# Optimization experiments

Measured on AMD Instinct MI355X. Metric: run time of the kernel, lower is better.

The kernel has to match this reference:

```python
import jax, jax.numpy as jnp
import numpy as np

OBS, ACT, HID, P, B = 128, 32, 256, 64, 4096
EPS = 1e-5


def _block(x, W, b, g, be, act=True):
    # x: [B, P, Din]; W: [P, Din, Dout]; b/g/be: [P, Dout]
    y = jnp.einsum('bpi,pio->bpo', x, W) + b
    # GroupNorm with one group per sub-policy: normalize over Dout per (b, p)
    mu = jnp.mean(y, axis=-1, keepdims=True)
    var = jnp.var(y, axis=-1, keepdims=True)
    y = (y - mu) * jax.lax.rsqrt(var + EPS) * g + be
    return jax.nn.elu(y) if act else y


def setup_inputs() -> dict:
    key = jax.random.key(0)
    ks = jax.random.split(key, 17)
    s = 0.05
    return {
        'observation': jax.random.normal(ks[0], (B, OBS), dtype=jnp.float32),
        'W1': jax.random.normal(ks[1], (P, OBS, HID), dtype=jnp.float32) * s,
        'b1': jax.random.normal(ks[2], (P, HID), dtype=jnp.float32) * s,
        'g1': jnp.ones((P, HID), dtype=jnp.float32),
        'be1': jnp.zeros((P, HID), dtype=jnp.float32),
        'W2': jax.random.normal(ks[3], (P, HID, HID), dtype=jnp.float32) * s,
        'b2': jax.random.normal(ks[4], (P, HID), dtype=jnp.float32) * s,
        'g2': jnp.ones((P, HID), dtype=jnp.float32),
        'be2': jnp.zeros((P, HID), dtype=jnp.float32),
        'W3': jax.random.normal(ks[5], (P, HID, HID), dtype=jnp.float32) * s,
        'b3': jax.random.normal(ks[6], (P, HID), dtype=jnp.float32) * s,
        'g3': jnp.ones((P, HID), dtype=jnp.float32),
        'be3': jnp.zeros((P, HID), dtype=jnp.float32),
        'W4': jax.random.normal(ks[7], (P, HID, ACT), dtype=jnp.float32) * s,
        'b4': jax.random.normal(ks[8], (P, ACT), dtype=jnp.float32) * s,
        'g4': jnp.ones((P, ACT), dtype=jnp.float32),
        'be4': jnp.zeros((P, ACT), dtype=jnp.float32),
    }


def reference(observation, W1, b1, g1, be1, W2, b2, g2, be2,
              W3, b3, g3, be3, W4, b4, g4, be4):
    # broadcast observation to each sub-policy: [B, P, OBS]
    x = jnp.broadcast_to(observation[:, None, :], (observation.shape[0], P, OBS))
    x = _block(x, W1, b1, g1, be1, act=True)
    x = _block(x, W2, b2, g2, be2, act=True)
    x = _block(x, W3, b3, g3, be3, act=True)
    x = _block(x, W4, b4, g4, be4, act=False)
    return x  # [B, P, ACT] action logits
```

## Files before the change

kernel.cpp:

```cpp
#include <hip/hip_runtime.h>

#define B_    4096
#define P_    64
#define OBS_  128
#define HID_  256
#define ACTD_ 32

typedef __attribute__((ext_vector_type(8)))  __bf16 bf16x8;
typedef __attribute__((ext_vector_type(2)))  __bf16 bf16x2_t;
typedef __attribute__((ext_vector_type(2)))  float  f32x2;
typedef __attribute__((ext_vector_type(4)))  float  f32x4;
typedef __attribute__((ext_vector_type(16))) float  f32x16;

#define XSTRIDE 264

#define WS1 0L
#define WS2 2097152L
#define WS3 6291456L
#define WS4 10485760L

#if defined(__has_builtin)
#if __has_builtin(__builtin_amdgcn_cvt_pk_bf16_f32)
#define HAVE_CVT_PK_BF16 1
#endif
#endif
#ifndef HAVE_CVT_PK_BF16
#define HAVE_CVT_PK_BF16 0
#endif

__device__ __forceinline__ unsigned short f2bf(float x) {
    unsigned u = __builtin_bit_cast(unsigned, x);
    u = (u + 0x7fffu + ((u >> 16) & 1u)) >> 16;
    return (unsigned short)u;
}

__device__ __forceinline__ unsigned pack_bf16_rne(float a, float b) {
#if HAVE_CVT_PK_BF16
    bf16x2_t p = __builtin_amdgcn_cvt_pk_bf16_f32(a, b);
    return __builtin_bit_cast(unsigned, p);
#else
    unsigned ua = __builtin_bit_cast(unsigned, a);
    unsigned ub = __builtin_bit_cast(unsigned, b);
    ua = ua + 0x7fffu + ((ua >> 16) & 1u);
    ub = ub + 0x7fffu + ((ub >> 16) & 1u);
    return __builtin_amdgcn_perm(ub, ua, 0x07060302u);
#endif
}

__device__ __forceinline__ void elu2_asm(float &a, float &b) {
    float ra, rb;
    asm volatile(
        "v_mul_f32 %0, 0x3fb8aa3b, %2\n\t"
        "v_mul_f32 %1, 0x3fb8aa3b, %3\n\t"
        "v_exp_f32 %0, %0\n\t"
        "v_exp_f32 %1, %1\n\t"
        "s_nop 0\n\t"
        "v_add_f32 %0, -1.0, %0\n\t"
        "v_add_f32 %1, -1.0, %1\n\t"
        "v_cmp_lt_f32 vcc, 0, %2\n\t"
        "v_cndmask_b32 %0, %0, %2, vcc\n\t"
        "v_cmp_lt_f32 vcc, 0, %3\n\t"
        "v_cndmask_b32 %1, %1, %3, vcc"
        : "=&v"(ra), "=&v"(rb) : "v"(a), "v"(b) : "vcc");
    a = ra; b = rb;
}

template<int K, int N, bool PERM>
__device__ __forceinline__ void prep_body(const float* __restrict__ W,
                                          unsigned short* __restrict__ out,
                                          int b, int t)
{
    constexpr int CH = K / 32;
    int tid  = b * 256 + t;
    int n    = tid % N;
    int rest = tid / N;
    int u    = rest % 4;
    rest    /= 4;
    int c    = rest % CH;
    int p    = rest / CH;
    unsigned short tmp[8];
#pragma unroll
    for (int j = 0; j < 8; ++j) {
        int sk = c * 32 + u * 8 + j;
        int k  = PERM ? ((sk & ~63) | ((sk & 1) << 5) | ((sk >> 1) & 31)) : sk;
        tmp[j] = f2bf(W[((long)(p * K + k)) * N + n]);
    }
    unsigned short* dst = out + ((((long)(p * CH + c) * 4 + u) * N + n) * 8);
    *reinterpret_cast<uint4*>(dst) = *reinterpret_cast<const uint4*>(tmp);
}

extern "C" __global__ __launch_bounds__(256)
void prep_all(const float* __restrict__ W1, const float* __restrict__ W2,
              const float* __restrict__ W3, const float* __restrict__ W4,
              unsigned short* __restrict__ ws)
{
    int b = blockIdx.x, t = threadIdx.x;
    if      (b < 1024) prep_body<128, 256, false>(W1, ws + WS1, b,        t);
    else if (b < 3072) prep_body<256, 256, true >(W2, ws + WS2, b - 1024, t);
    else if (b < 5120) prep_body<256, 256, true >(W3, ws + WS3, b - 3072, t);
    else               prep_body<256, 32,  true >(W4, ws + WS4, b - 5120, t);
}

template<int KCH>
__device__ __forceinline__ void layer256(
    unsigned short* __restrict__ X,
    const char* __restrict__ wsrc,
    const float* __restrict__ bp, const float* __restrict__ gp, const float* __restrict__ bep,
    float2* __restrict__ part, float2* __restrict__ stats,
    int tid, bool elu)
{
    const int w  = tid >> 6;
    const int l5 = tid & 31;
    const int h  = (tid & 63) >> 5;

    const bf16x8* __restrict__ Bp = (const bf16x8*)wsrc + (h * 256 + w * 64 + l5);

    f32x16 acc[2][2];
#pragma unroll
    for (int rt = 0; rt < 2; ++rt)
#pragma unroll
        for (int ct = 0; ct < 2; ++ct)
#pragma unroll
            for (int r = 0; r < 16; ++r) acc[rt][ct][r] = 0.f;

#pragma unroll
    for (int c = 0; c < KCH; ++c) {
        const int k0 = c * 16 + h * 8;
        bf16x8 a0 = *(const bf16x8*)(X + l5 * XSTRIDE + k0);
        bf16x8 a1 = *(const bf16x8*)(X + (32 + l5) * XSTRIDE + k0);
        bf16x8 b0 = Bp[c * 512];
        bf16x8 b1 = Bp[c * 512 + 32];
        acc[0][0] = __builtin_amdgcn_mfma_f32_32x32x16_bf16(a0, b0, acc[0][0], 0, 0, 0);
        acc[1][0] = __builtin_amdgcn_mfma_f32_32x32x16_bf16(a1, b0, acc[1][0], 0, 0, 0);
        acc[0][1] = __builtin_amdgcn_mfma_f32_32x32x16_bf16(a0, b1, acc[0][1], 0, 0, 0);
        acc[1][1] = __builtin_amdgcn_mfma_f32_32x32x16_bf16(a1, b1, acc[1][1], 0, 0, 0);
    }
    __syncthreads();

    const int n0 = w * 64 + l5, n1 = n0 + 32;
    const int pos = w * 64 + 2 * l5;
    const f32x2 bias2 = {bp[n0], bp[n1]};
#pragma unroll
    for (int rt = 0; rt < 2; ++rt)
#pragma unroll
        for (int r = 0; r < 16; ++r) {
            f32x2 t = {acc[rt][0][r], acc[rt][1][r]};
            t += bias2;
            acc[rt][0][r] = t.x; acc[rt][1][r] = t.y;
        }

#pragma unroll
    for (int rt = 0; rt < 2; ++rt)
#pragma unroll
        for (int r = 0; r < 16; ++r) {
            const int row = rt * 32 + (r & 3) + 8 * (r >> 2) + 4 * h;
            *reinterpret_cast<unsigned*>(X + row * XSTRIDE + pos) =
                pack_bf16_rne(acc[rt][0][r], acc[rt][1][r]);
        }

    {
        const int lane = tid & 63;
        f32x2 S = {0.f, 0.f}, S2 = {0.f, 0.f};
#pragma unroll
        for (int j8 = 0; j8 < 8; ++j8) {
            bf16x8 v8 = *(const bf16x8*)(X + lane * XSTRIDE + w * 64 + j8 * 8);
#pragma unroll
            for (int e = 0; e < 4; ++e) {
                f32x2 vv = {(float)v8[2 * e], (float)v8[2 * e + 1]};
                S += vv;
                S2 = vv * vv + S2;
            }
        }
        part[lane * 4 + w] = make_float2(S.x + S.y, S2.x + S2.y);
    }
    __syncthreads();
    if (w == 0) {
        const int lane = tid & 63;
        float2 p0 = part[lane * 4 + 0], p1 = part[lane * 4 + 1];
        float2 p2 = part[lane * 4 + 2], p3 = part[lane * 4 + 3];
        float s  = p0.x + p1.x + p2.x + p3.x;
        float s2 = p0.y + p1.y + p2.y + p3.y;
        float mu  = s * (1.f / 256.f);
        float var = s2 * (1.f / 256.f) - mu * mu;
        stats[lane] = make_float2(mu, rsqrtf(var + 1e-5f));
    }
    __syncthreads();

    const f32x2 gv2  = {gp[n0], gp[n1]};
    const f32x2 bev2 = {bep[n0], bep[n1]};
#pragma unroll
    for (int rt = 0; rt < 2; ++rt)
#pragma unroll
        for (int r = 0; r < 16; ++r) {
            const int row = rt * 32 + (r & 3) + 8 * (r >> 2) + 4 * h;
            float2 st = stats[row];
            f32x2 mu2 = {st.x, st.x};
            f32x2 rs2 = {st.y, st.y};
            f32x2 yv  = {acc[rt][0][r], acc[rt][1][r]};
            f32x2 zv  = (yv - mu2) * rs2 * gv2 + bev2;
            float v0 = zv.x, v1 = zv.y;
            if (elu) elu2_asm(v0, v1);
            *reinterpret_cast<unsigned*>(X + row * XSTRIDE + pos) = pack_bf16_rne(v0, v1);
        }
    __syncthreads();
}

__device__ __forceinline__ void layer32(
    const unsigned short* __restrict__ X,
    const char* __restrict__ wsrc,
    const float* __restrict__ bp, const float* __restrict__ gp, const float* __restrict__ bep,
    float* __restrict__ outg, int bbase, int p, int tid)
{
    const int w = tid >> 6, lane = tid & 63, ln = lane & 15, quad = lane >> 4;
    const bf16x8* __restrict__ Bp = (const bf16x8*)wsrc + (quad * 32 + ln);

    f32x4 acc[2];
#pragma unroll
    for (int nt = 0; nt < 2; ++nt)
#pragma unroll
        for (int r = 0; r < 4; ++r) acc[nt][r] = 0.f;

#pragma unroll
    for (int c = 0; c < 8; ++c) {
        bf16x8 a  = *(const bf16x8*)(X + (16 * w + ln) * XSTRIDE + c * 32 + quad * 8);
        bf16x8 b0 = Bp[c * 128];
        bf16x8 b1 = Bp[c * 128 + 16];
        acc[0] = __builtin_amdgcn_mfma_f32_16x16x32_bf16(a, b0, acc[0], 0, 0, 0);
        acc[1] = __builtin_amdgcn_mfma_f32_16x16x32_bf16(a, b1, acc[1], 0, 0, 0);
    }

    const float bb0 = bp[ln], bb1 = bp[16 + ln];
    const float g0 = gp[ln], g1 = gp[16 + ln], be0 = bep[ln], be1 = bep[16 + ln];
#pragma unroll
    for (int r = 0; r < 4; ++r) {
        float y0 = acc[0][r] + bb0, y1 = acc[1][r] + bb1;
        float s = y0 + y1, s2 = y0 * y0 + y1 * y1;
        s += __shfl_xor(s, 1);  s2 += __shfl_xor(s2, 1);
        s += __shfl_xor(s, 2);  s2 += __shfl_xor(s2, 2);
        s += __shfl_xor(s, 4);  s2 += __shfl_xor(s2, 4);
        s += __shfl_xor(s, 8);  s2 += __shfl_xor(s2, 8);
        float mu  = s * (1.f / 32.f);
        float var = s2 * (1.f / 32.f) - mu * mu;
        float rs  = rsqrtf(var + 1e-5f);
        const int row = bbase + 16 * w + quad * 4 + r;
        float* o = outg + ((long)row * P_ + p) * ACTD_;
        o[ln]      = (y0 - mu) * rs * g0 + be0;
        o[16 + ln] = (y1 - mu) * rs * g1 + be1;
    }
}

extern "C" __global__ void __launch_bounds__(256, 4)
policy_fused(const float* __restrict__ obs,
             const unsigned short* __restrict__ wbf,
             const float* __restrict__ b1, const float* __restrict__ g1, const float* __restrict__ be1,
             const float* __restrict__ b2, const float* __restrict__ g2, const float* __restrict__ be2,
             const float* __restrict__ b3, const float* __restrict__ g3, const float* __restrict__ be3,
             const float* __restrict__ b4, const float* __restrict__ g4, const float* __restrict__ be4,
             float* __restrict__ out)
{
    __shared__ __align__(16) unsigned short X[64 * XSTRIDE];
    __shared__ float2 part[64 * 4];
    __shared__ float2 stats[64];

    const int tid = threadIdx.x;
    const int bx  = blockIdx.x;
    const int p     = ((bx & 7) << 3) | ((bx >> 3) & 7);
    const int bbase = (bx >> 6) * 64;

    const char* ws1 = (const char*)(wbf + WS1 + (long)p * (128 * 256));
    const char* ws2 = (const char*)(wbf + WS2 + (long)p * (256 * 256));
    const char* ws3 = (const char*)(wbf + WS3 + (long)p * (256 * 256));
    const char* ws4 = (const char*)(wbf + WS4 + (long)p * (256 * 32));

    for (int idx = tid; idx < 64 * 32; idx += 256) {
        int row = idx >> 5, c4 = idx & 31;
        float4 v = *reinterpret_cast<const float4*>(obs + (long)(bbase + row) * OBS_ + c4 * 4);
        uint2 pk;
        pk.x = pack_bf16_rne(v.x, v.y);
        pk.y = pack_bf16_rne(v.z, v.w);
        *reinterpret_cast<uint2*>(X + row * XSTRIDE + c4 * 4) = pk;
    }
    __syncthreads();

    layer256<8>(X, ws1, b1 + p * 256, g1 + p * 256, be1 + p * 256, part, stats, tid, true);
    layer256<16>(X, ws2, b2 + p * 256, g2 + p * 256, be2 + p * 256, part, stats, tid, true);
    layer256<16>(X, ws3, b3 + p * 256, g3 + p * 256, be3 + p * 256, part, stats, tid, true);
    layer32(X, ws4, b4 + p * 32, g4 + p * 32, be4 + p * 32, out, bbase, p, tid);
}

extern "C" void kernel_launch(void* const* d_in, const int* in_sizes, int n_in,
                              void* d_out, int out_size, void* d_ws, size_t ws_size,
                              hipStream_t stream)
{
    const float* obs = (const float*)d_in[0];
    const float* W1  = (const float*)d_in[1];
    const float* b1  = (const float*)d_in[2];
    const float* g1  = (const float*)d_in[3];
    const float* be1 = (const float*)d_in[4];
    const float* W2  = (const float*)d_in[5];
    const float* b2  = (const float*)d_in[6];
    const float* g2  = (const float*)d_in[7];
    const float* be2 = (const float*)d_in[8];
    const float* W3  = (const float*)d_in[9];
    const float* b3  = (const float*)d_in[10];
    const float* g3  = (const float*)d_in[11];
    const float* be3 = (const float*)d_in[12];
    const float* W4  = (const float*)d_in[13];
    const float* b4  = (const float*)d_in[14];
    const float* g4  = (const float*)d_in[15];
    const float* be4 = (const float*)d_in[16];
    float* out = (float*)d_out;
    unsigned short* ws = (unsigned short*)d_ws;

    hipLaunchKernelGGL(prep_all, dim3(5376), dim3(256), 0, stream, W1, W2, W3, W4, ws);

    hipLaunchKernelGGL(policy_fused, dim3(4096), dim3(256), 0, stream,
                       obs, ws,
                       b1, g1, be1, b2, g2, be2, b3, g3, be3, b4, g4, be4, out);
}
```

Baseline: 279.1 us.

## Swap MFMA operands so accumulators are row-major and compute GroupNorm stats in registers

The 256-wide layers now pass weights as the A operand and activations as B, so each lane holds contiguous output columns for one batch row. That lets the GroupNorm sums be taken straight from the accumulators, which removes the bf16 round-trip through shared memory, and outputs are written as 8-byte stores. The bias is folded into the accumulator initialisation, and the k-permutation in weight prep is dropped to match the new operand order. The partial-sum buffer grows to 64x9 float2, and the final layer also gets bias-in-accumulator initialisation.

```diff
diff --git a/kernel.cpp b/kernel.cpp
--- a/kernel.cpp
+++ b/kernel.cpp
@@ -8,7 +8,6 @@
 
 typedef __attribute__((ext_vector_type(8)))  __bf16 bf16x8;
 typedef __attribute__((ext_vector_type(2)))  __bf16 bf16x2_t;
-typedef __attribute__((ext_vector_type(2)))  float  f32x2;
 typedef __attribute__((ext_vector_type(4)))  float  f32x4;
 typedef __attribute__((ext_vector_type(16))) float  f32x16;
 
@@ -65,7 +64,7 @@
     a = ra; b = rb;
 }
 
-template<int K, int N, bool PERM>
+template<int K, int N>
 __device__ __forceinline__ void prep_body(const float* __restrict__ W,
                                           unsigned short* __restrict__ out,
                                           int b, int t)
@@ -78,13 +77,11 @@
     rest    /= 4;
     int c    = rest % CH;
     int p    = rest / CH;
+    const float* __restrict__ src = W + ((long)(p * K + c * 32 + u * 8)) * N + n;
     unsigned short tmp[8];
 #pragma unroll
-    for (int j = 0; j < 8; ++j) {
-        int sk = c * 32 + u * 8 + j;
-        int k  = PERM ? ((sk & ~63) | ((sk & 1) << 5) | ((sk >> 1) & 31)) : sk;
-        tmp[j] = f2bf(W[((long)(p * K + k)) * N + n]);
-    }
+    for (int j = 0; j < 8; ++j)
+        tmp[j] = f2bf(src[(long)j * N]);
     unsigned short* dst = out + ((((long)(p * CH + c) * 4 + u) * N + n) * 8);
     *reinterpret_cast<uint4*>(dst) = *reinterpret_cast<const uint4*>(tmp);
 }
@@ -95,10 +92,10 @@
               unsigned short* __restrict__ ws)
 {
     int b = blockIdx.x, t = threadIdx.x;
-    if      (b < 1024) prep_body<128, 256, false>(W1, ws + WS1, b,        t);
-    else if (b < 3072) prep_body<256, 256, true >(W2, ws + WS2, b - 1024, t);
-    else if (b < 5120) prep_body<256, 256, true >(W3, ws + WS3, b - 3072, t);
-    else               prep_body<256, 32,  true >(W4, ws + WS4, b - 5120, t);
+    if      (b < 1024) prep_body<128, 256>(W1, ws + WS1, b,        t);
+    else if (b < 3072) prep_body<256, 256>(W2, ws + WS2, b - 1024, t);
+    else if (b < 5120) prep_body<256, 256>(W3, ws + WS3, b - 3072, t);
+    else               prep_body<256, 32 >(W4, ws + WS4, b - 5120, t);
 }
 
 template<int KCH>
@@ -113,95 +110,89 @@
     const int l5 = tid & 31;
     const int h  = (tid & 63) >> 5;
 
-    const bf16x8* __restrict__ Bp = (const bf16x8*)wsrc + (h * 256 + w * 64 + l5);
+    const bf16x8* __restrict__ Wp = (const bf16x8*)wsrc + (h * 256 + w * 64 + l5);
+    const int nb = w * 64 + 4 * h;
 
     f32x16 acc[2][2];
 #pragma unroll
-    for (int rt = 0; rt < 2; ++rt)
-#pragma unroll
-        for (int ct = 0; ct < 2; ++ct)
-#pragma unroll
-            for (int r = 0; r < 16; ++r) acc[rt][ct][r] = 0.f;
+    for (int nt = 0; nt < 2; ++nt)
+#pragma unroll
+        for (int q = 0; q < 4; ++q) {
+            const float4 b4 = *reinterpret_cast<const float4*>(bp + nb + nt * 32 + 8 * q);
+#pragma unroll
+            for (int mt = 0; mt < 2; ++mt) {
+                acc[nt][mt][4 * q + 0] = b4.x;
+                acc[nt][mt][4 * q + 1] = b4.y;
+                acc[nt][mt][4 * q + 2] = b4.z;
+                acc[nt][mt][4 * q + 3] = b4.w;
+            }
+        }
 
 #pragma unroll
     for (int c = 0; c < KCH; ++c) {
         const int k0 = c * 16 + h * 8;
-        bf16x8 a0 = *(const bf16x8*)(X + l5 * XSTRIDE + k0);
-        bf16x8 a1 = *(const bf16x8*)(X + (32 + l5) * XSTRIDE + k0);
-        bf16x8 b0 = Bp[c * 512];
-        bf16x8 b1 = Bp[c * 512 + 32];
-        acc[0][0] = __builtin_amdgcn_mfma_f32_32x32x16_bf16(a0, b0, acc[0][0], 0, 0, 0);
-        acc[1][0] = __builtin_amdgcn_mfma_f32_32x32x16_bf16(a1, b0, acc[1][0], 0, 0, 0);
-        acc[0][1] = __builtin_amdgcn_mfma_f32_32x32x16_bf16(a0, b1, acc[0][1], 0, 0, 0);
-        acc[1][1] = __builtin_amdgcn_mfma_f32_32x32x16_bf16(a1, b1, acc[1][1], 0, 0, 0);
-    }
-    __syncthreads();
-
-    const int n0 = w * 64 + l5, n1 = n0 + 32;
-    const int pos = w * 64 + 2 * l5;
-    const f32x2 bias2 = {bp[n0], bp[n1]};
-#pragma unroll
-    for (int rt = 0; rt < 2; ++rt)
+        bf16x8 x0 = *(const bf16x8*)(X + l5 * XSTRIDE + k0);
+        bf16x8 x1 = *(const bf16x8*)(X + (32 + l5) * XSTRIDE + k0);
+        bf16x8 w0 = Wp[c * 512];
+        bf16x8 w1 = Wp[c * 512 + 32];
+        acc[0][0] = __builtin_amdgcn_mfma_f32_32x32x16_bf16(w0, x0, acc[0][0], 0, 0, 0);
+        acc[0][1] = __builtin_amdgcn_mfma_f32_32x32x16_bf16(w0, x1, acc[0][1], 0, 0, 0);
+        acc[1][0] = __builtin_amdgcn_mfma_f32_32x32x16_bf16(w1, x0, acc[1][0], 0, 0, 0);
+        acc[1][1] = __builtin_amdgcn_mfma_f32_32x32x16_bf16(w1, x1, acc[1][1], 0, 0, 0);
+    }
+    __syncthreads();
+
+    float s0 = 0.f, s20 = 0.f, s1 = 0.f, s21 = 0.f;
+#pragma unroll
+    for (int nt = 0; nt < 2; ++nt)
 #pragma unroll
         for (int r = 0; r < 16; ++r) {
-            f32x2 t = {acc[rt][0][r], acc[rt][1][r]};
-            t += bias2;
-            acc[rt][0][r] = t.x; acc[rt][1][r] = t.y;
+            float v0 = acc[nt][0][r];
+            float v1 = acc[nt][1][r];
+            s0 += v0;  s20 = fmaf(v0, v0, s20);
+            s1 += v1;  s21 = fmaf(v1, v1, s21);
         }
-
-#pragma unroll
-    for (int rt = 0; rt < 2; ++rt)
-#pragma unroll
-        for (int r = 0; r < 16; ++r) {
-            const int row = rt * 32 + (r & 3) + 8 * (r >> 2) + 4 * h;
-            *reinterpret_cast<unsigned*>(X + row * XSTRIDE + pos) =
-                pack_bf16_rne(acc[rt][0][r], acc[rt][1][r]);
-        }
-
-    {
-        const int lane = tid & 63;
-        f32x2 S = {0.f, 0.f}, S2 = {0.f, 0.f};
-#pragma unroll
-        for (int j8 = 0; j8 < 8; ++j8) {
-            bf16x8 v8 = *(const bf16x8*)(X + lane * XSTRIDE + w * 64 + j8 * 8);
-#pragma unroll
-            for (int e = 0; e < 4; ++e) {
-                f32x2 vv = {(float)v8[2 * e], (float)v8[2 * e + 1]};
-                S += vv;
-                S2 = vv * vv + S2;
-            }
-        }
-        part[lane * 4 + w] = make_float2(S.x + S.y, S2.x + S2.y);
-    }
+    part[l5 * 9 + w * 2 + h]        = make_float2(s0, s20);
+    part[(32 + l5) * 9 + w * 2 + h] = make_float2(s1, s21);
     __syncthreads();
     if (w == 0) {
         const int lane = tid & 63;
-        float2 p0 = part[lane * 4 + 0], p1 = part[lane * 4 + 1];
-        float2 p2 = part[lane * 4 + 2], p3 = part[lane * 4 + 3];
-        float s  = p0.x + p1.x + p2.x + p3.x;
-        float s2 = p0.y + p1.y + p2.y + p3.y;
+        float s = 0.f, s2 = 0.f;
+#pragma unroll
+        for (int i = 0; i < 8; ++i) {
+            float2 pp = part[lane * 9 + i];
+            s += pp.x; s2 += pp.y;
+        }
         float mu  = s * (1.f / 256.f);
         float var = s2 * (1.f / 256.f) - mu * mu;
         stats[lane] = make_float2(mu, rsqrtf(var + 1e-5f));
     }
     __syncthreads();
 
-    const f32x2 gv2  = {gp[n0], gp[n1]};
-    const f32x2 bev2 = {bep[n0], bep[n1]};
-#pragma unroll
-    for (int rt = 0; rt < 2; ++rt)
-#pragma unroll
-        for (int r = 0; r < 16; ++r) {
-            const int row = rt * 32 + (r & 3) + 8 * (r >> 2) + 4 * h;
-            float2 st = stats[row];
-            f32x2 mu2 = {st.x, st.x};
-            f32x2 rs2 = {st.y, st.y};
-            f32x2 yv  = {acc[rt][0][r], acc[rt][1][r]};
-            f32x2 zv  = (yv - mu2) * rs2 * gv2 + bev2;
-            float v0 = zv.x, v1 = zv.y;
-            if (elu) elu2_asm(v0, v1);
-            *reinterpret_cast<unsigned*>(X + row * XSTRIDE + pos) = pack_bf16_rne(v0, v1);
+    const float2 st0 = stats[l5], st1 = stats[32 + l5];
+#pragma unroll
+    for (int nt = 0; nt < 2; ++nt) {
+#pragma unroll
+        for (int q = 0; q < 4; ++q) {
+            const int nq = nb + nt * 32 + 8 * q;
+            const float4 g4 = *reinterpret_cast<const float4*>(gp  + nq);
+            const float4 e4 = *reinterpret_cast<const float4*>(bep + nq);
+#pragma unroll
+            for (int mt = 0; mt < 2; ++mt) {
+                const float mu = mt ? st1.x : st0.x;
+                const float rs = mt ? st1.y : st0.y;
+                float v0 = (acc[nt][mt][4 * q + 0] - mu) * rs * g4.x + e4.x;
+                float v1 = (acc[nt][mt][4 * q + 1] - mu) * rs * g4.y + e4.y;
+                float v2 = (acc[nt][mt][4 * q + 2] - mu) * rs * g4.z + e4.z;
+                float v3 = (acc[nt][mt][4 * q + 3] - mu) * rs * g4.w + e4.w;
+                if (elu) { elu2_asm(v0, v1); elu2_asm(v2, v3); }
+                uint2 pk;
+                pk.x = pack_bf16_rne(v0, v1);
+                pk.y = pack_bf16_rne(v2, v3);
+                *reinterpret_cast<uint2*>(X + (mt * 32 + l5) * XSTRIDE + nq) = pk;
+            }
         }
+    }
     __syncthreads();
 }
 
@@ -214,11 +205,10 @@
     const int w = tid >> 6, lane = tid & 63, ln = lane & 15, quad = lane >> 4;
     const bf16x8* __restrict__ Bp = (const bf16x8*)wsrc + (quad * 32 + ln);
 
+    const float bb0 = bp[ln], bb1 = bp[16 + ln];
     f32x4 acc[2];
 #pragma unroll
-    for (int nt = 0; nt < 2; ++nt)
-#pragma unroll
-        for (int r = 0; r < 4; ++r) acc[nt][r] = 0.f;
+    for (int r = 0; r < 4; ++r) { acc[0][r] = bb0; acc[1][r] = bb1; }
 
 #pragma unroll
     for (int c = 0; c < 8; ++c) {
@@ -229,11 +219,10 @@
         acc[1] = __builtin_amdgcn_mfma_f32_16x16x32_bf16(a, b1, acc[1], 0, 0, 0);
     }
 
-    const float bb0 = bp[ln], bb1 = bp[16 + ln];
     const float g0 = gp[ln], g1 = gp[16 + ln], be0 = bep[ln], be1 = bep[16 + ln];
 #pragma unroll
     for (int r = 0; r < 4; ++r) {
-        float y0 = acc[0][r] + bb0, y1 = acc[1][r] + bb1;
+        float y0 = acc[0][r], y1 = acc[1][r];
         float s = y0 + y1, s2 = y0 * y0 + y1 * y1;
         s += __shfl_xor(s, 1);  s2 += __shfl_xor(s2, 1);
         s += __shfl_xor(s, 2);  s2 += __shfl_xor(s2, 2);
@@ -259,7 +248,7 @@
              float* __restrict__ out)
 {
     __shared__ __align__(16) unsigned short X[64 * XSTRIDE];
-    __shared__ float2 part[64 * 4];
+    __shared__ float2 part[64 * 9];
     __shared__ float2 stats[64];
 
     const int tid = threadIdx.x;
```

After: 259.4 us. -7.0%, faster.
